# Kernel optimization log

Hardware: AMD Instinct MI355X
Metric: run time of the kernel (lower is better)

Reference implementation:

```python
import jax, jax.numpy as jnp
import numpy as np

E, TOPK, C = 8, 2, 1  # num_local_experts, num_experts_per_tok, num_channels
BS, L, D, F = 8, 1024, 1024, 4096


def setup_inputs() -> dict:
    key = jax.random.key(0)
    ks = jax.random.split(key, 5)
    s = lambda fan_in: 1.0 / np.sqrt(fan_in)
    return {
        "hidden_states": jax.random.normal(ks[0], (BS, L, D), jnp.float32),
        # nn.Linear weight layout [out, in]
        "router_w": jax.random.normal(ks[1], (E, D * C), jnp.float32) * s(D * C),
        "w1": jax.random.normal(ks[2], (E, F, D), jnp.float32) * s(D),
        "w2": jax.random.normal(ks[3], (E, D, F), jnp.float32) * s(F),
        "w3": jax.random.normal(ks[4], (E, F, D), jnp.float32) * s(D),
    }


def _forward(hidden_states, router_w, w1, w2, w3):
    bs, seq, d = hidden_states.shape  # 3D path -> c = 1
    c = C
    h = hidden_states.reshape(bs, seq, c * d)  # [bs, L, c*d]
    # router: per-position logits, then mean over sequence (sentence-level routing)
    router_logits = jnp.einsum('blf,ef->ble', h, router_w).mean(axis=1)  # [bs, E]
    router_probs = jax.nn.softmax(router_logits, axis=-1)
    topk_w, topk_idx = jax.lax.top_k(router_probs, TOPK)  # [bs, TOPK]

    # dense all-expert SwiGLU MLP on every token (as in the original)
    x = h.reshape(bs, seq, c, d)
    outs = []
    for e in range(E):  # fixed small expert count
        up = jnp.einsum('blcd,fd->blcf', x, w1[e])
        gate = jnp.einsum('blcd,fd->blcf', x, w3[e])
        y = jnp.einsum('blcf,df->blcd', jax.nn.silu(up) * gate, w2[e])
        outs.append(y.reshape(bs, seq, c * d))
    expert_outputs = jnp.stack(outs, axis=1)  # [bs, E, L, c*d]

    # Faithful replication of torch.gather(dim=1) with index [bs,L,TOPK,h]:
    # out[b,l,j,:] = expert_outputs[b, topk_idx[b,j], j, :]  (independent of l)
    bi = jnp.arange(bs)[:, None]
    ji = jnp.arange(TOPK)[None, :]
    sel = expert_outputs[bi, topk_idx, ji]  # [bs, TOPK, c*d]
    combined = (sel * topk_w[..., None]).sum(axis=1)  # [bs, c*d]
    out = jnp.broadcast_to(combined[:, None, :], (bs, seq, c * d))
    out = out.reshape(bs, c, seq, d)
    return out, router_logits


def reference(hidden_states, router_w, w1, w2, w3):
    return _forward(hidden_states, router_w, w1, w2, w3)
```

## Files before the change

kernel.cpp:

```cpp
#include <hip/hip_runtime.h>
#include <math.h>

#define BS 8
#define SEQ 1024
#define DIM 1024
#define FF 4096
#define NE 8
#define NSLOT 16
#define MAXM 8
#define NCHUNK 64

#define KS_UG 2
#define KR_UG (DIM / KS_UG)
#define KS_DN 16
#define KR_DN (FF / KS_DN)

#define WS_LPART 0
#define WS_SELW  (WS_LPART + BS*NCHUNK*NE)
#define WS_SELE  (WS_SELW + NSLOT)
#define WS_ACT   (WS_SELE + NSLOT)
#define WS_UPP   (WS_ACT + NSLOT*FF)
#define WS_GTP   (WS_UPP + KS_UG*NSLOT*FF)
#define WS_YP    WS_UPP
#define WS_Y     (WS_GTP + KS_UG*NSLOT*FF)

__device__ __forceinline__ float dot4(float4 a, float4 b) {
    return a.x*b.x + a.y*b.y + a.z*b.z + a.w*b.w;
}

__global__ __launch_bounds__(256) void klogit(const float4* __restrict__ h4,
                                              const float4* __restrict__ rw4,
                                              float* __restrict__ lpart) {
    const int c = blockIdx.x, b = blockIdx.y, t = threadIdx.x;
    const float4* p = h4 + ((size_t)b * SEQ + (size_t)c * 16) * (DIM/4) + t;
    float4 s = make_float4(0.f, 0.f, 0.f, 0.f);
    #pragma unroll
    for (int i = 0; i < 16; ++i) {
        float4 v = p[(size_t)i * (DIM/4)];
        s.x += v.x; s.y += v.y; s.z += v.z; s.w += v.w;
    }
    __shared__ float red[4];
    const int wave = t >> 6, lane = t & 63;
    for (int e = 0; e < NE; ++e) {
        float pd = dot4(s, rw4[(size_t)e * (DIM/4) + t]);
        #pragma unroll
        for (int o = 32; o; o >>= 1) pd += __shfl_xor(pd, o);
        if (lane == 0) red[wave] = pd;
        __syncthreads();
        if (t == 0) lpart[(size_t)(b * NCHUNK + c) * NE + e] = red[0]+red[1]+red[2]+red[3];
        __syncthreads();
    }
}

__global__ void krouter2(const float* __restrict__ lpart,
                         float* __restrict__ out_logits,
                         float* __restrict__ selw, int* __restrict__ sele) {
    const int t = threadIdx.x;
    __shared__ float lg[BS * NE];
    if (t < BS * NE) {
        const int b = t >> 3, e = t & 7;
        float s = 0.f;
        for (int c = 0; c < NCHUNK; ++c) s += lpart[(size_t)(b * NCHUNK + c) * NE + e];
        s *= (1.0f / (float)SEQ);
        lg[b * NE + e] = s;
        out_logits[b * NE + e] = s;
    }
    __syncthreads();
    if (t < BS) {
        float l[NE]; float mx = -1e30f;
        #pragma unroll
        for (int e = 0; e < NE; ++e) { l[e] = lg[t * NE + e]; mx = fmaxf(mx, l[e]); }
        float sum = 0.f;
        #pragma unroll
        for (int e = 0; e < NE; ++e) { l[e] = expf(l[e] - mx); sum += l[e]; }
        const float invs = 1.f / sum;
        float v1 = -1.f, v2 = -1.f; int e1 = -1, e2 = -1;
        #pragma unroll
        for (int e = 0; e < NE; ++e) {
            float pe = l[e] * invs;
            if (pe > v1)      { v2 = v1; e2 = e1; v1 = pe; e1 = e; }
            else if (pe > v2) { v2 = pe; e2 = e; }
        }
        selw[t * 2 + 0] = v1; sele[t * 2 + 0] = e1;
        selw[t * 2 + 1] = v2; sele[t * 2 + 1] = e2;
    }
}

__device__ __forceinline__ int build_slots(const int* __restrict__ sele, int e, int* slot) {
    unsigned mask = 0;
    #pragma unroll
    for (int s = 0; s < NSLOT; ++s) mask |= (sele[s] == e) ? (1u << s) : 0u;
    const int m = __popc(mask);
    unsigned mm = mask;
    #pragma unroll
    for (int ti = 0; ti < MAXM; ++ti) { slot[ti] = __ffs(mm) - 1; mm &= mm - 1; }
    return m;
}

template<int M>
__device__ void ug_body(const float4* __restrict__ wp, const float* __restrict__ xs,
                        float* __restrict__ outp, const int* slot, int row, int sub) {
    float acc[M];
    #pragma unroll
    for (int ti = 0; ti < M; ++ti) acc[ti] = 0.f;
    #pragma unroll 4
    for (int g = 0; g < KR_UG / 16; ++g) {
        float4 w = wp[g * 4];
        #pragma unroll
        for (int ti = 0; ti < M; ++ti) {
            float4 x = *(const float4*)(xs + ti * KR_UG + g * 16 + sub * 4);
            acc[ti] += dot4(w, x);
        }
    }
    #pragma unroll
    for (int ti = 0; ti < M; ++ti) {
        float v = acc[ti];
        v += __shfl_xor(v, 1); v += __shfl_xor(v, 2);
        if (sub == 0) outp[(size_t)slot[ti] * FF + row] = v;
    }
}

__global__ __launch_bounds__(256) void kupgate(const float* __restrict__ h,
                                               const float* __restrict__ w1,
                                               const float* __restrict__ w3,
                                               const int* __restrict__ sele,
                                               float* __restrict__ upp,
                                               float* __restrict__ gtp) {
    __shared__ float xs[MAXM * KR_UG];
    const int tile = blockIdx.x, e = blockIdx.y;
    const int mat = blockIdx.z & 1, ks = blockIdx.z >> 1;
    int slot[MAXM];
    const int m = build_slots(sele, e, slot);
    if (m == 0) return;
    {
        const int ti = threadIdx.x >> 5, j = threadIdx.x & 31;
        if (ti < m) {
            const int s = slot[ti];
            const float4* src = (const float4*)(h
                + ((size_t)((s >> 1) * SEQ + (s & 1))) * DIM + ks * KR_UG);
            float4* dst = (float4*)(xs + ti * KR_UG);
            #pragma unroll
            for (int i = 0; i < KR_UG / 128; ++i) dst[j + i * 32] = src[j + i * 32];
        }
    }
    __syncthreads();
    const int lane = threadIdx.x & 63, wave = threadIdx.x >> 6;
    const int sub = lane & 3;
    const int row = tile * 64 + wave * 16 + (lane >> 2);
    const float* wmat = (mat ? w3 : w1) + (size_t)e * FF * DIM;
    const float4* wp = (const float4*)(wmat + (size_t)row * DIM + ks * KR_UG) + sub;
    float* outp = (mat ? gtp : upp) + (size_t)ks * NSLOT * FF;
    switch (m) {
        case 1: ug_body<1>(wp, xs, outp, slot, row, sub); break;
        case 2: ug_body<2>(wp, xs, outp, slot, row, sub); break;
        case 3: ug_body<3>(wp, xs, outp, slot, row, sub); break;
        case 4: ug_body<4>(wp, xs, outp, slot, row, sub); break;
        case 5: ug_body<5>(wp, xs, outp, slot, row, sub); break;
        case 6: ug_body<6>(wp, xs, outp, slot, row, sub); break;
        case 7: ug_body<7>(wp, xs, outp, slot, row, sub); break;
        default: ug_body<8>(wp, xs, outp, slot, row, sub); break;
    }
}

__global__ __launch_bounds__(256) void kact(const float* __restrict__ upp,
                                            const float* __restrict__ gtp,
                                            float* __restrict__ act) {
    const int r = blockIdx.x * 256 + threadIdx.x, s = blockIdx.y;
    float u = 0.f, g = 0.f;
    #pragma unroll
    for (int ks = 0; ks < KS_UG; ++ks) {
        u += upp[((size_t)ks * NSLOT + s) * FF + r];
        g += gtp[((size_t)ks * NSLOT + s) * FF + r];
    }
    act[(size_t)s * FF + r] = (u / (1.f + expf(-u))) * g;
}

template<int M>
__device__ void dn_body(const float4* __restrict__ wp, const float* __restrict__ xs,
                        float* __restrict__ outp, const int* slot, int row, int sub) {
    float acc[M];
    #pragma unroll
    for (int ti = 0; ti < M; ++ti) acc[ti] = 0.f;
    #pragma unroll 4
    for (int g = 0; g < KR_DN / 16; ++g) {
        float4 w = wp[g * 4];
        #pragma unroll
        for (int ti = 0; ti < M; ++ti) {
            float4 x = *(const float4*)(xs + ti * KR_DN + g * 16 + sub * 4);
            acc[ti] += dot4(w, x);
        }
    }
    #pragma unroll
    for (int ti = 0; ti < M; ++ti) {
        float v = acc[ti];
        v += __shfl_xor(v, 1); v += __shfl_xor(v, 2);
        if (sub == 0) outp[(size_t)slot[ti] * DIM + row] = v;
    }
}

__global__ __launch_bounds__(256) void kdown(const float* __restrict__ w2,
                                             const float* __restrict__ act,
                                             const int* __restrict__ sele,
                                             float* __restrict__ yp) {
    __shared__ float xs[MAXM * KR_DN];
    const int tile = blockIdx.x, e = blockIdx.y, ks = blockIdx.z;
    int slot[MAXM];
    const int m = build_slots(sele, e, slot);
    if (m == 0) return;
    {
        const int ti = threadIdx.x >> 5, j = threadIdx.x & 31;
        if (ti < m) {
            const float4* src = (const float4*)(act + (size_t)slot[ti] * FF + ks * KR_DN);
            float4* dst = (float4*)(xs + ti * KR_DN);
            #pragma unroll
            for (int i = 0; i < KR_DN / 128; ++i) dst[j + i * 32] = src[j + i * 32];
        }
    }
    __syncthreads();
    const int lane = threadIdx.x & 63, wave = threadIdx.x >> 6;
    const int sub = lane & 3;
    const int row = tile * 64 + wave * 16 + (lane >> 2);
    const float4* wp = (const float4*)(w2 + (size_t)e * DIM * FF
                                       + (size_t)row * FF + ks * KR_DN) + sub;
    float* outp = yp + (size_t)ks * NSLOT * DIM;
    switch (m) {
        case 1: dn_body<1>(wp, xs, outp, slot, row, sub); break;
        case 2: dn_body<2>(wp, xs, outp, slot, row, sub); break;
        case 3: dn_body<3>(wp, xs, outp, slot, row, sub); break;
        case 4: dn_body<4>(wp, xs, outp, slot, row, sub); break;
        case 5: dn_body<5>(wp, xs, outp, slot, row, sub); break;
        case 6: dn_body<6>(wp, xs, outp, slot, row, sub); break;
        case 7: dn_body<7>(wp, xs, outp, slot, row, sub); break;
        default: dn_body<8>(wp, xs, outp, slot, row, sub); break;
    }
}

__global__ __launch_bounds__(256) void kcomb(const float* __restrict__ yp,
                                             const float* __restrict__ selw,
                                             float* __restrict__ y) {
    const int r = blockIdx.x * 256 + threadIdx.x, s = blockIdx.y;
    float v = 0.f;
    #pragma unroll
    for (int ks = 0; ks < KS_DN; ++ks)
        v += yp[((size_t)ks * NSLOT + s) * DIM + r];
    y[(size_t)s * DIM + r] = selw[s] * v;
}

__global__ __launch_bounds__(256) void kbcast(const float4* __restrict__ y4,
                                              float4* __restrict__ out4) {
    const int b = blockIdx.y, lg = blockIdx.x, t = threadIdx.x;
    float4 y0 = y4[(size_t)(2 * b) * (DIM/4) + t];
    float4 y1 = y4[(size_t)(2 * b + 1) * (DIM/4) + t];
    float4 c = make_float4(y0.x + y1.x, y0.y + y1.y, y0.z + y1.z, y0.w + y1.w);
    size_t base = ((size_t)b * SEQ + (size_t)lg * 8) * (DIM/4) + t;
    #pragma unroll
    for (int i = 0; i < 8; ++i) out4[base + (size_t)i * (DIM/4)] = c;
}

extern "C" void kernel_launch(void* const* d_in, const int* in_sizes, int n_in,
                              void* d_out, int out_size, void* d_ws, size_t ws_size,
                              hipStream_t stream) {
    const float* h  = (const float*)d_in[0];
    const float* rw = (const float*)d_in[1];
    const float* w1 = (const float*)d_in[2];
    const float* w2 = (const float*)d_in[3];
    const float* w3 = (const float*)d_in[4];
    float* out = (float*)d_out;
    float* ws  = (float*)d_ws;

    float* lpart = ws + WS_LPART;
    float* selw  = ws + WS_SELW;
    int*   sele  = (int*)(ws + WS_SELE);
    float* act   = ws + WS_ACT;
    float* upp   = ws + WS_UPP;
    float* gtp   = ws + WS_GTP;
    float* yp    = ws + WS_YP;
    float* y     = ws + WS_Y;
    float* out_logits = out + (size_t)BS * SEQ * DIM;

    klogit  <<<dim3(NCHUNK, BS), 256, 0, stream>>>((const float4*)h, (const float4*)rw, lpart);
    krouter2<<<1, 64, 0, stream>>>(lpart, out_logits, selw, sele);
    kupgate <<<dim3(FF / 64, NE, 2 * KS_UG), 256, 0, stream>>>(h, w1, w3, sele, upp, gtp);
    kact    <<<dim3(FF / 256, NSLOT), 256, 0, stream>>>(upp, gtp, act);
    kdown   <<<dim3(DIM / 64, NE, KS_DN), 256, 0, stream>>>(w2, act, sele, yp);
    kcomb   <<<dim3(DIM / 256, NSLOT), 256, 0, stream>>>(yp, selw, y);
    kbcast  <<<dim3(SEQ / 8, BS), 256, 0, stream>>>((const float4*)y, (float4*)out);
}
```

Baseline: 120.2 us.

## Fuse up/gate/SiLU into one kernel and drop split-K partials for down projection

Merges the up/gate GEMV, partial reduction and SiLU activation into a single kernel in which each wave owns whole rows of w1 and w3, reduces across the full K dimension and writes the activated value directly. The down projection likewise computes over the full FF dimension inside one block, staging activation chunks through shared memory, and applies the routing weight on output, which removes the separate combine kernel. This removes two launches and the partial-sum workspace round trips, and adds register double-buffering of weight loads. In exchange there are fewer blocks per launch and more work per block, which may reduce memory-level parallelism for these bandwidth-bound weight reads.

```diff
diff --git a/kernel.cpp b/kernel.cpp
--- a/kernel.cpp
+++ b/kernel.cpp
@@ -10,19 +10,11 @@
 #define MAXM 8
 #define NCHUNK 64
 
-#define KS_UG 2
-#define KR_UG (DIM / KS_UG)
-#define KS_DN 16
-#define KR_DN (FF / KS_DN)
-
 #define WS_LPART 0
 #define WS_SELW  (WS_LPART + BS*NCHUNK*NE)
 #define WS_SELE  (WS_SELW + NSLOT)
 #define WS_ACT   (WS_SELE + NSLOT)
-#define WS_UPP   (WS_ACT + NSLOT*FF)
-#define WS_GTP   (WS_UPP + KS_UG*NSLOT*FF)
-#define WS_YP    WS_UPP
-#define WS_Y     (WS_GTP + KS_UG*NSLOT*FF)
+#define WS_Y     (WS_ACT + NSLOT*FF)
 
 __device__ __forceinline__ float dot4(float4 a, float4 b) {
     return a.x*b.x + a.y*b.y + a.z*b.z + a.w*b.w;
@@ -97,153 +89,167 @@
     return m;
 }
 
-template<int M>
-__device__ void ug_body(const float4* __restrict__ wp, const float* __restrict__ xs,
-                        float* __restrict__ outp, const int* slot, int row, int sub) {
-    float acc[M];
-    #pragma unroll
-    for (int ti = 0; ti < M; ++ti) acc[ti] = 0.f;
-    #pragma unroll 4
-    for (int g = 0; g < KR_UG / 16; ++g) {
-        float4 w = wp[g * 4];
-        #pragma unroll
-        for (int ti = 0; ti < M; ++ti) {
-            float4 x = *(const float4*)(xs + ti * KR_UG + g * 16 + sub * 4);
-            acc[ti] += dot4(w, x);
-        }
-    }
-    #pragma unroll
-    for (int ti = 0; ti < M; ++ti) {
-        float v = acc[ti];
-        v += __shfl_xor(v, 1); v += __shfl_xor(v, 2);
-        if (sub == 0) outp[(size_t)slot[ti] * FF + row] = v;
-    }
-}
-
-__global__ __launch_bounds__(256) void kupgate(const float* __restrict__ h,
+#define SW_LD(Ar, Br, R8) {                                            \
+    const size_t rb_ = (size_t)(rowbase + (R8)) * 256 + lane;          \
+    _Pragma("unroll")                                                  \
+    for (int i_ = 0; i_ < 4; ++i_) {                                   \
+        Ar[i_] = w1e4[rb_ + i_ * 64];                                  \
+        Br[i_] = w3e4[rb_ + i_ * 64];                                  \
+    } }
+
+template<int MM>
+__device__ void swiglu_body(const float4* __restrict__ w1e4,
+                            const float4* __restrict__ w3e4,
+                            const float4* __restrict__ xs4,
+                            float* __restrict__ act,
+                            const int* slot, int m, int rowbase, int lane) {
+    float4 A0[4], B0[4], A1[4], B1[4];
+    SW_LD(A0, B0, 0)
+    for (int r8 = 0; r8 < 8; r8 += 2) {
+        SW_LD(A1, B1, r8 + 1)
+        {
+            const int row = rowbase + r8;
+            #pragma unroll
+            for (int ti = 0; ti < MM; ++ti) {
+                float u = 0.f, g = 0.f;
+                #pragma unroll
+                for (int i = 0; i < 4; ++i) {
+                    float4 x = xs4[ti * 256 + i * 64 + lane];
+                    u += dot4(A0[i], x); g += dot4(B0[i], x);
+                }
+                #pragma unroll
+                for (int o = 32; o; o >>= 1) { u += __shfl_xor(u, o); g += __shfl_xor(g, o); }
+                if (ti < m && lane == 0)
+                    act[(size_t)slot[ti] * FF + row] = (u / (1.f + expf(-u))) * g;
+            }
+        }
+        if (r8 + 2 < 8) SW_LD(A0, B0, r8 + 2)
+        {
+            const int row = rowbase + r8 + 1;
+            #pragma unroll
+            for (int ti = 0; ti < MM; ++ti) {
+                float u = 0.f, g = 0.f;
+                #pragma unroll
+                for (int i = 0; i < 4; ++i) {
+                    float4 x = xs4[ti * 256 + i * 64 + lane];
+                    u += dot4(A1[i], x); g += dot4(B1[i], x);
+                }
+                #pragma unroll
+                for (int o = 32; o; o >>= 1) { u += __shfl_xor(u, o); g += __shfl_xor(g, o); }
+                if (ti < m && lane == 0)
+                    act[(size_t)slot[ti] * FF + row] = (u / (1.f + expf(-u))) * g;
+            }
+        }
+    }
+}
+
+__global__ __launch_bounds__(256) void kswiglu(const float* __restrict__ h,
                                                const float* __restrict__ w1,
                                                const float* __restrict__ w3,
                                                const int* __restrict__ sele,
-                                               float* __restrict__ upp,
-                                               float* __restrict__ gtp) {
-    __shared__ float xs[MAXM * KR_UG];
-    const int tile = blockIdx.x, e = blockIdx.y;
-    const int mat = blockIdx.z & 1, ks = blockIdx.z >> 1;
+                                               float* __restrict__ act) {
+    __shared__ float xs[MAXM * DIM];
+    const int tile = blockIdx.x, e = blockIdx.y, t = threadIdx.x;
     int slot[MAXM];
     const int m = build_slots(sele, e, slot);
     if (m == 0) return;
     {
-        const int ti = threadIdx.x >> 5, j = threadIdx.x & 31;
+        const int ti = t >> 5, j = t & 31;
+        float4* dst = (float4*)(xs + ti * DIM);
         if (ti < m) {
             const int s = slot[ti];
-            const float4* src = (const float4*)(h
-                + ((size_t)((s >> 1) * SEQ + (s & 1))) * DIM + ks * KR_UG);
-            float4* dst = (float4*)(xs + ti * KR_UG);
-            #pragma unroll
-            for (int i = 0; i < KR_UG / 128; ++i) dst[j + i * 32] = src[j + i * 32];
+            const float4* src = (const float4*)(h + ((size_t)((s >> 1) * SEQ + (s & 1))) * DIM);
+            #pragma unroll
+            for (int i = 0; i < 8; ++i) dst[j + i * 32] = src[j + i * 32];
+        } else {
+            const float4 z = make_float4(0.f, 0.f, 0.f, 0.f);
+            #pragma unroll
+            for (int i = 0; i < 8; ++i) dst[j + i * 32] = z;
         }
     }
     __syncthreads();
-    const int lane = threadIdx.x & 63, wave = threadIdx.x >> 6;
-    const int sub = lane & 3;
-    const int row = tile * 64 + wave * 16 + (lane >> 2);
-    const float* wmat = (mat ? w3 : w1) + (size_t)e * FF * DIM;
-    const float4* wp = (const float4*)(wmat + (size_t)row * DIM + ks * KR_UG) + sub;
-    float* outp = (mat ? gtp : upp) + (size_t)ks * NSLOT * FF;
-    switch (m) {
-        case 1: ug_body<1>(wp, xs, outp, slot, row, sub); break;
-        case 2: ug_body<2>(wp, xs, outp, slot, row, sub); break;
-        case 3: ug_body<3>(wp, xs, outp, slot, row, sub); break;
-        case 4: ug_body<4>(wp, xs, outp, slot, row, sub); break;
-        case 5: ug_body<5>(wp, xs, outp, slot, row, sub); break;
-        case 6: ug_body<6>(wp, xs, outp, slot, row, sub); break;
-        case 7: ug_body<7>(wp, xs, outp, slot, row, sub); break;
-        default: ug_body<8>(wp, xs, outp, slot, row, sub); break;
-    }
-}
-
-__global__ __launch_bounds__(256) void kact(const float* __restrict__ upp,
-                                            const float* __restrict__ gtp,
-                                            float* __restrict__ act) {
-    const int r = blockIdx.x * 256 + threadIdx.x, s = blockIdx.y;
-    float u = 0.f, g = 0.f;
-    #pragma unroll
-    for (int ks = 0; ks < KS_UG; ++ks) {
-        u += upp[((size_t)ks * NSLOT + s) * FF + r];
-        g += gtp[((size_t)ks * NSLOT + s) * FF + r];
-    }
-    act[(size_t)s * FF + r] = (u / (1.f + expf(-u))) * g;
-}
-
-template<int M>
-__device__ void dn_body(const float4* __restrict__ wp, const float* __restrict__ xs,
-                        float* __restrict__ outp, const int* slot, int row, int sub) {
-    float acc[M];
-    #pragma unroll
-    for (int ti = 0; ti < M; ++ti) acc[ti] = 0.f;
-    #pragma unroll 4
-    for (int g = 0; g < KR_DN / 16; ++g) {
-        float4 w = wp[g * 4];
-        #pragma unroll
-        for (int ti = 0; ti < M; ++ti) {
-            float4 x = *(const float4*)(xs + ti * KR_DN + g * 16 + sub * 4);
-            acc[ti] += dot4(w, x);
-        }
-    }
-    #pragma unroll
-    for (int ti = 0; ti < M; ++ti) {
-        float v = acc[ti];
-        v += __shfl_xor(v, 1); v += __shfl_xor(v, 2);
-        if (sub == 0) outp[(size_t)slot[ti] * DIM + row] = v;
+    const int wave = t >> 6, lane = t & 63;
+    const int rowbase = tile * 32 + wave * 8;
+    const float4* w1e4 = (const float4*)w1 + (size_t)e * FF * (DIM/4);
+    const float4* w3e4 = (const float4*)w3 + (size_t)e * FF * (DIM/4);
+    if (m <= 4) swiglu_body<4>(w1e4, w3e4, (const float4*)xs, act, slot, m, rowbase, lane);
+    else        swiglu_body<8>(w1e4, w3e4, (const float4*)xs, act, slot, m, rowbase, lane);
+}
+
+template<int MM>
+__device__ void down_body(const float4* __restrict__ w2e4,
+                          const float* __restrict__ act,
+                          const float* __restrict__ selw,
+                          float* __restrict__ y,
+                          const int* slot, int m, int tile, int t, float* xs) {
+    const int wave = t >> 6, lane = t & 63;
+    const int rowbase = tile * 16 + wave * 4;
+    float acc[4][MM];
+    #pragma unroll
+    for (int r = 0; r < 4; ++r)
+        #pragma unroll
+        for (int ti = 0; ti < MM; ++ti) acc[r][ti] = 0.f;
+
+    for (int c = 0; c < 4; ++c) {
+        __syncthreads();
+        {
+            const int ti = t >> 5, j = t & 31;
+            float4* dst = (float4*)(xs + ti * 1024);
+            if (ti < m) {
+                const float4* src = (const float4*)(act + (size_t)slot[ti] * FF + c * 1024);
+                #pragma unroll
+                for (int i = 0; i < 8; ++i) dst[j + i * 32] = src[j + i * 32];
+            } else {
+                const float4 z = make_float4(0.f, 0.f, 0.f, 0.f);
+                #pragma unroll
+                for (int i = 0; i < 8; ++i) dst[j + i * 32] = z;
+            }
+        }
+        __syncthreads();
+        float4 W[4][4];
+        #pragma unroll
+        for (int r = 0; r < 4; ++r) {
+            const size_t rb = (size_t)(rowbase + r) * (FF/4) + c * 256 + lane;
+            #pragma unroll
+            for (int i = 0; i < 4; ++i) W[r][i] = w2e4[rb + i * 64];
+        }
+        const float4* xs4 = (const float4*)xs;
+        #pragma unroll
+        for (int i = 0; i < 4; ++i) {
+            #pragma unroll
+            for (int ti = 0; ti < MM; ++ti) {
+                float4 x = xs4[ti * 256 + i * 64 + lane];
+                #pragma unroll
+                for (int r = 0; r < 4; ++r) acc[r][ti] += dot4(W[r][i], x);
+            }
+        }
+    }
+    #pragma unroll
+    for (int r = 0; r < 4; ++r) {
+        #pragma unroll
+        for (int ti = 0; ti < MM; ++ti) {
+            float v = acc[r][ti];
+            #pragma unroll
+            for (int o = 32; o; o >>= 1) v += __shfl_xor(v, o);
+            if (ti < m && lane == 0)
+                y[(size_t)slot[ti] * DIM + rowbase + r] = selw[slot[ti]] * v;
+        }
     }
 }
 
 __global__ __launch_bounds__(256) void kdown(const float* __restrict__ w2,
                                              const float* __restrict__ act,
                                              const int* __restrict__ sele,
-                                             float* __restrict__ yp) {
-    __shared__ float xs[MAXM * KR_DN];
-    const int tile = blockIdx.x, e = blockIdx.y, ks = blockIdx.z;
+                                             const float* __restrict__ selw,
+                                             float* __restrict__ y) {
+    __shared__ float xs[MAXM * 1024];
+    const int tile = blockIdx.x, e = blockIdx.y, t = threadIdx.x;
     int slot[MAXM];
     const int m = build_slots(sele, e, slot);
     if (m == 0) return;
-    {
-        const int ti = threadIdx.x >> 5, j = threadIdx.x & 31;
-        if (ti < m) {
-            const float4* src = (const float4*)(act + (size_t)slot[ti] * FF + ks * KR_DN);
-            float4* dst = (float4*)(xs + ti * KR_DN);
-            #pragma unroll
-            for (int i = 0; i < KR_DN / 128; ++i) dst[j + i * 32] = src[j + i * 32];
-        }
-    }
-    __syncthreads();
-    const int lane = threadIdx.x & 63, wave = threadIdx.x >> 6;
-    const int sub = lane & 3;
-    const int row = tile * 64 + wave * 16 + (lane >> 2);
-    const float4* wp = (const float4*)(w2 + (size_t)e * DIM * FF
-                                       + (size_t)row * FF + ks * KR_DN) + sub;
-    float* outp = yp + (size_t)ks * NSLOT * DIM;
-    switch (m) {
-        case 1: dn_body<1>(wp, xs, outp, slot, row, sub); break;
-        case 2: dn_body<2>(wp, xs, outp, slot, row, sub); break;
-        case 3: dn_body<3>(wp, xs, outp, slot, row, sub); break;
-        case 4: dn_body<4>(wp, xs, outp, slot, row, sub); break;
-        case 5: dn_body<5>(wp, xs, outp, slot, row, sub); break;
-        case 6: dn_body<6>(wp, xs, outp, slot, row, sub); break;
-        case 7: dn_body<7>(wp, xs, outp, slot, row, sub); break;
-        default: dn_body<8>(wp, xs, outp, slot, row, sub); break;
-    }
-}
-
-__global__ __launch_bounds__(256) void kcomb(const float* __restrict__ yp,
-                                             const float* __restrict__ selw,
-                                             float* __restrict__ y) {
-    const int r = blockIdx.x * 256 + threadIdx.x, s = blockIdx.y;
-    float v = 0.f;
-    #pragma unroll
-    for (int ks = 0; ks < KS_DN; ++ks)
-        v += yp[((size_t)ks * NSLOT + s) * DIM + r];
-    y[(size_t)s * DIM + r] = selw[s] * v;
+    const float4* w2e4 = (const float4*)w2 + (size_t)e * DIM * (FF/4);
+    if (m <= 4) down_body<4>(w2e4, act, selw, y, slot, m, tile, t, xs);
+    else        down_body<8>(w2e4, act, selw, y, slot, m, tile, t, xs);
 }
 
 __global__ __launch_bounds__(256) void kbcast(const float4* __restrict__ y4,
@@ -272,17 +278,12 @@
     float* selw  = ws + WS_SELW;
     int*   sele  = (int*)(ws + WS_SELE);
     float* act   = ws + WS_ACT;
-    float* upp   = ws + WS_UPP;
-    float* gtp   = ws + WS_GTP;
-    float* yp    = ws + WS_YP;
     float* y     = ws + WS_Y;
     float* out_logits = out + (size_t)BS * SEQ * DIM;
 
     klogit  <<<dim3(NCHUNK, BS), 256, 0, stream>>>((const float4*)h, (const float4*)rw, lpart);
     krouter2<<<1, 64, 0, stream>>>(lpart, out_logits, selw, sele);
-    kupgate <<<dim3(FF / 64, NE, 2 * KS_UG), 256, 0, stream>>>(h, w1, w3, sele, upp, gtp);
-    kact    <<<dim3(FF / 256, NSLOT), 256, 0, stream>>>(upp, gtp, act);
-    kdown   <<<dim3(DIM / 64, NE, KS_DN), 256, 0, stream>>>(w2, act, sele, yp);
-    kcomb   <<<dim3(DIM / 256, NSLOT), 256, 0, stream>>>(yp, selw, y);
+    kswiglu <<<dim3(FF / 32, NE), 256, 0, stream>>>(h, w1, w3, sele, act);
+    kdown   <<<dim3(DIM / 16, NE), 256, 0, stream>>>(w2, act, sele, selw, y);
     kbcast  <<<dim3(SEQ / 8, BS), 256, 0, stream>>>((const float4*)y, (float4*)out);
 }
```

Measured after the change: 127.1 us. 5.7% more time.

## Fuse up/gate GEMV, map one weight row per thread, batch router reductions

Applied to the files above, without the earlier changes.

The up and gate projections are merged into one kernel, so each block streams both w1 and w3 rows and reuses the staged token vectors held in shared memory. Both GEMV kernels switch from four lanes sharing a row to one full row per thread, which removes the cross-lane shuffle reduction. They also collapse the eight templated slot counts into two variants (4 and 8), and the up/gate K-split goes from 2 to 4. The router logit kernel now reduces all eight experts together with one barrier instead of two barriers per expert. The costs are that adjacent lanes now read weight rows a full row apart, which loses coalescing, and that padded slots do wasted FMAs when m is not 4 or 8.

```diff
diff --git a/kernel.cpp b/kernel.cpp
--- a/kernel.cpp
+++ b/kernel.cpp
@@ -10,10 +10,10 @@
 #define MAXM 8
 #define NCHUNK 64
 
-#define KS_UG 2
-#define KR_UG (DIM / KS_UG)
+#define KS_UG 4
+#define KC_UG (DIM / KS_UG)
 #define KS_DN 16
-#define KR_DN (FF / KS_DN)
+#define KC_DN (FF / KS_DN)
 
 #define WS_LPART 0
 #define WS_SELW  (WS_LPART + BS*NCHUNK*NE)
@@ -39,17 +39,24 @@
         float4 v = p[(size_t)i * (DIM/4)];
         s.x += v.x; s.y += v.y; s.z += v.z; s.w += v.w;
     }
-    __shared__ float red[4];
+    float pd[NE];
+    #pragma unroll
+    for (int e = 0; e < NE; ++e) pd[e] = dot4(s, rw4[(size_t)e * (DIM/4) + t]);
+    #pragma unroll
+    for (int o = 32; o; o >>= 1) {
+        #pragma unroll
+        for (int e = 0; e < NE; ++e) pd[e] += __shfl_xor(pd[e], o);
+    }
+    __shared__ float red[4][NE];
     const int wave = t >> 6, lane = t & 63;
-    for (int e = 0; e < NE; ++e) {
-        float pd = dot4(s, rw4[(size_t)e * (DIM/4) + t]);
-        #pragma unroll
-        for (int o = 32; o; o >>= 1) pd += __shfl_xor(pd, o);
-        if (lane == 0) red[wave] = pd;
-        __syncthreads();
-        if (t == 0) lpart[(size_t)(b * NCHUNK + c) * NE + e] = red[0]+red[1]+red[2]+red[3];
-        __syncthreads();
-    }
+    if (lane == 0) {
+        #pragma unroll
+        for (int e = 0; e < NE; ++e) red[wave][e] = pd[e];
+    }
+    __syncthreads();
+    if (t < NE)
+        lpart[(size_t)(b * NCHUNK + c) * NE + t] =
+            red[0][t] + red[1][t] + red[2][t] + red[3][t];
 }
 
 __global__ void krouter2(const float* __restrict__ lpart,
@@ -97,69 +104,89 @@
     return m;
 }
 
-template<int M>
-__device__ void ug_body(const float4* __restrict__ wp, const float* __restrict__ xs,
-                        float* __restrict__ outp, const int* slot, int row, int sub) {
-    float acc[M];
-    #pragma unroll
-    for (int ti = 0; ti < M; ++ti) acc[ti] = 0.f;
-    #pragma unroll 4
-    for (int g = 0; g < KR_UG / 16; ++g) {
-        float4 w = wp[g * 4];
-        #pragma unroll
-        for (int ti = 0; ti < M; ++ti) {
-            float4 x = *(const float4*)(xs + ti * KR_UG + g * 16 + sub * 4);
-            acc[ti] += dot4(w, x);
-        }
-    }
-    #pragma unroll
-    for (int ti = 0; ti < M; ++ti) {
-        float v = acc[ti];
-        v += __shfl_xor(v, 1); v += __shfl_xor(v, 2);
-        if (sub == 0) outp[(size_t)slot[ti] * FF + row] = v;
-    }
-}
-
-__global__ __launch_bounds__(256) void kupgate(const float* __restrict__ h,
+__device__ __forceinline__ void slots_to_lds(const int* __restrict__ sele, int e,
+                                             int t, int* sslot) {
+    if (t < MAXM) {
+        unsigned mask = 0;
+        #pragma unroll
+        for (int s = 0; s < NSLOT; ++s) mask |= (sele[s] == e) ? (1u << s) : 0u;
+        unsigned mm = mask; int sl = -1;
+        for (int k = 0; k <= t; ++k) { sl = __ffs(mm) - 1; mm &= mm - 1; }
+        sslot[t] = sl;
+    }
+}
+
+template<int MM>
+__device__ void swiglu_body(const float4* __restrict__ w1p,
+                            const float4* __restrict__ w3p,
+                            const float4* __restrict__ xs4,
+                            float* __restrict__ up_out, float* __restrict__ gt_out,
+                            const int* slot, int m, int row) {
+    float ua[MM], ga[MM];
+    #pragma unroll
+    for (int ti = 0; ti < MM; ++ti) { ua[ti] = 0.f; ga[ti] = 0.f; }
+    for (int c = 0; c < KC_UG / 16; ++c) {
+        float4 W1[4], W3[4];
+        #pragma unroll
+        for (int i = 0; i < 4; ++i) W1[i] = w1p[c * 4 + i];
+        #pragma unroll
+        for (int i = 0; i < 4; ++i) W3[i] = w3p[c * 4 + i];
+        #pragma unroll
+        for (int i = 0; i < 4; ++i) {
+            #pragma unroll
+            for (int ti = 0; ti < MM; ++ti) {
+                float4 x = xs4[ti * (KC_UG/4) + c * 4 + i];
+                ua[ti] += dot4(W1[i], x);
+                ga[ti] += dot4(W3[i], x);
+            }
+        }
+    }
+    #pragma unroll
+    for (int ti = 0; ti < MM; ++ti) {
+        if (ti < m) {
+            up_out[(size_t)slot[ti] * FF + row] = ua[ti];
+            gt_out[(size_t)slot[ti] * FF + row] = ga[ti];
+        }
+    }
+}
+
+__global__ __launch_bounds__(256) void kswiglu(const float* __restrict__ h,
                                                const float* __restrict__ w1,
                                                const float* __restrict__ w3,
                                                const int* __restrict__ sele,
                                                float* __restrict__ upp,
                                                float* __restrict__ gtp) {
-    __shared__ float xs[MAXM * KR_UG];
-    const int tile = blockIdx.x, e = blockIdx.y;
-    const int mat = blockIdx.z & 1, ks = blockIdx.z >> 1;
+    __shared__ float xs[MAXM * KC_UG];
+    __shared__ int sslot[MAXM];
+    const int tile = blockIdx.x, e = blockIdx.y, ks = blockIdx.z, t = threadIdx.x;
     int slot[MAXM];
     const int m = build_slots(sele, e, slot);
     if (m == 0) return;
+    slots_to_lds(sele, e, t, sslot);
+    __syncthreads();
     {
-        const int ti = threadIdx.x >> 5, j = threadIdx.x & 31;
-        if (ti < m) {
-            const int s = slot[ti];
-            const float4* src = (const float4*)(h
-                + ((size_t)((s >> 1) * SEQ + (s & 1))) * DIM + ks * KR_UG);
-            float4* dst = (float4*)(xs + ti * KR_UG);
-            #pragma unroll
-            for (int i = 0; i < KR_UG / 128; ++i) dst[j + i * 32] = src[j + i * 32];
-        }
-    }
-    __syncthreads();
-    const int lane = threadIdx.x & 63, wave = threadIdx.x >> 6;
-    const int sub = lane & 3;
-    const int row = tile * 64 + wave * 16 + (lane >> 2);
-    const float* wmat = (mat ? w3 : w1) + (size_t)e * FF * DIM;
-    const float4* wp = (const float4*)(wmat + (size_t)row * DIM + ks * KR_UG) + sub;
-    float* outp = (mat ? gtp : upp) + (size_t)ks * NSLOT * FF;
-    switch (m) {
-        case 1: ug_body<1>(wp, xs, outp, slot, row, sub); break;
-        case 2: ug_body<2>(wp, xs, outp, slot, row, sub); break;
-        case 3: ug_body<3>(wp, xs, outp, slot, row, sub); break;
-        case 4: ug_body<4>(wp, xs, outp, slot, row, sub); break;
-        case 5: ug_body<5>(wp, xs, outp, slot, row, sub); break;
-        case 6: ug_body<6>(wp, xs, outp, slot, row, sub); break;
-        case 7: ug_body<7>(wp, xs, outp, slot, row, sub); break;
-        default: ug_body<8>(wp, xs, outp, slot, row, sub); break;
-    }
+        float4* xs4 = (float4*)xs;
+        const float4* h4 = (const float4*)h;
+        #pragma unroll
+        for (int q = 0; q < 2; ++q) {
+            const int idx = t + q * 256;
+            const int ti = idx >> 6, j = idx & 63;
+            const int s = sslot[ti];
+            float4 v = make_float4(0.f, 0.f, 0.f, 0.f);
+            if (ti < m)
+                v = h4[((size_t)((s >> 1) * SEQ + (s & 1))) * (DIM/4) + ks * (KC_UG/4) + j];
+            xs4[idx] = v;
+        }
+    }
+    __syncthreads();
+    const int wave = t >> 6, lane = t & 63;
+    const int row = tile * 256 + wave * 64 + lane;
+    const float4* w1p = (const float4*)w1 + ((size_t)e * FF + row) * (DIM/4) + ks * (KC_UG/4);
+    const float4* w3p = (const float4*)w3 + ((size_t)e * FF + row) * (DIM/4) + ks * (KC_UG/4);
+    float* up_out = upp + (size_t)ks * NSLOT * FF;
+    float* gt_out = gtp + (size_t)ks * NSLOT * FF;
+    if (m <= 4) swiglu_body<4>(w1p, w3p, (const float4*)xs, up_out, gt_out, slot, m, row);
+    else        swiglu_body<8>(w1p, w3p, (const float4*)xs, up_out, gt_out, slot, m, row);
 }
 
 __global__ __launch_bounds__(256) void kact(const float* __restrict__ upp,
@@ -175,69 +202,69 @@
     act[(size_t)s * FF + r] = (u / (1.f + expf(-u))) * g;
 }
 
-template<int M>
-__device__ void dn_body(const float4* __restrict__ wp, const float* __restrict__ xs,
-                        float* __restrict__ outp, const int* slot, int row, int sub) {
-    float acc[M];
-    #pragma unroll
-    for (int ti = 0; ti < M; ++ti) acc[ti] = 0.f;
-    #pragma unroll 4
-    for (int g = 0; g < KR_DN / 16; ++g) {
-        float4 w = wp[g * 4];
-        #pragma unroll
-        for (int ti = 0; ti < M; ++ti) {
-            float4 x = *(const float4*)(xs + ti * KR_DN + g * 16 + sub * 4);
-            acc[ti] += dot4(w, x);
-        }
-    }
-    #pragma unroll
-    for (int ti = 0; ti < M; ++ti) {
-        float v = acc[ti];
-        v += __shfl_xor(v, 1); v += __shfl_xor(v, 2);
-        if (sub == 0) outp[(size_t)slot[ti] * DIM + row] = v;
-    }
+template<int MM>
+__device__ void down_body(const float4* __restrict__ wp,
+                          const float4* __restrict__ xs4,
+                          float* __restrict__ y_out,
+                          const int* slot, int m, int row) {
+    float acc[MM];
+    #pragma unroll
+    for (int ti = 0; ti < MM; ++ti) acc[ti] = 0.f;
+    for (int c = 0; c < KC_DN / 16; ++c) {
+        float4 W[4];
+        #pragma unroll
+        for (int i = 0; i < 4; ++i) W[i] = wp[c * 4 + i];
+        #pragma unroll
+        for (int i = 0; i < 4; ++i) {
+            #pragma unroll
+            for (int ti = 0; ti < MM; ++ti) {
+                float4 x = xs4[ti * (KC_DN/4) + c * 4 + i];
+                acc[ti] += dot4(W[i], x);
+            }
+        }
+    }
+    #pragma unroll
+    for (int ti = 0; ti < MM; ++ti)
+        if (ti < m) y_out[(size_t)slot[ti] * DIM + row] = acc[ti];
 }
 
 __global__ __launch_bounds__(256) void kdown(const float* __restrict__ w2,
                                              const float* __restrict__ act,
                                              const int* __restrict__ sele,
                                              float* __restrict__ yp) {
-    __shared__ float xs[MAXM * KR_DN];
-    const int tile = blockIdx.x, e = blockIdx.y, ks = blockIdx.z;
+    __shared__ float xs[MAXM * KC_DN];
+    __shared__ int sslot[MAXM];
+    const int tile = blockIdx.x, e = blockIdx.y, ks = blockIdx.z, t = threadIdx.x;
     int slot[MAXM];
     const int m = build_slots(sele, e, slot);
     if (m == 0) return;
+    slots_to_lds(sele, e, t, sslot);
+    __syncthreads();
     {
-        const int ti = threadIdx.x >> 5, j = threadIdx.x & 31;
-        if (ti < m) {
-            const float4* src = (const float4*)(act + (size_t)slot[ti] * FF + ks * KR_DN);
-            float4* dst = (float4*)(xs + ti * KR_DN);
-            #pragma unroll
-            for (int i = 0; i < KR_DN / 128; ++i) dst[j + i * 32] = src[j + i * 32];
-        }
-    }
-    __syncthreads();
-    const int lane = threadIdx.x & 63, wave = threadIdx.x >> 6;
-    const int sub = lane & 3;
-    const int row = tile * 64 + wave * 16 + (lane >> 2);
-    const float4* wp = (const float4*)(w2 + (size_t)e * DIM * FF
-                                       + (size_t)row * FF + ks * KR_DN) + sub;
-    float* outp = yp + (size_t)ks * NSLOT * DIM;
-    switch (m) {
-        case 1: dn_body<1>(wp, xs, outp, slot, row, sub); break;
-        case 2: dn_body<2>(wp, xs, outp, slot, row, sub); break;
-        case 3: dn_body<3>(wp, xs, outp, slot, row, sub); break;
-        case 4: dn_body<4>(wp, xs, outp, slot, row, sub); break;
-        case 5: dn_body<5>(wp, xs, outp, slot, row, sub); break;
-        case 6: dn_body<6>(wp, xs, outp, slot, row, sub); break;
-        case 7: dn_body<7>(wp, xs, outp, slot, row, sub); break;
-        default: dn_body<8>(wp, xs, outp, slot, row, sub); break;
-    }
-}
-
-__global__ __launch_bounds__(256) void kcomb(const float* __restrict__ yp,
-                                             const float* __restrict__ selw,
-                                             float* __restrict__ y) {
+        float4* xs4 = (float4*)xs;
+        const float4* a4 = (const float4*)act;
+        #pragma unroll
+        for (int q = 0; q < 2; ++q) {
+            const int idx = t + q * 256;
+            const int ti = idx >> 6, j = idx & 63;
+            const int s = sslot[ti];
+            float4 v = make_float4(0.f, 0.f, 0.f, 0.f);
+            if (ti < m) v = a4[(size_t)s * (FF/4) + ks * (KC_DN/4) + j];
+            xs4[idx] = v;
+        }
+    }
+    __syncthreads();
+    const int wave = t >> 6, lane = t & 63;
+    const int row = tile * 256 + wave * 64 + lane;
+    const float4* wp = (const float4*)w2 + ((size_t)e * DIM + row) * (FF/4) + ks * (KC_DN/4);
+    float* y_out = yp + (size_t)ks * NSLOT * DIM;
+    if (m <= 4) down_body<4>(wp, (const float4*)xs, y_out, slot, m, row);
+    else        down_body<8>(wp, (const float4*)xs, y_out, slot, m, row);
+}
+
+__global__ __launch_bounds__(256) void kcomby(const float* __restrict__ yp,
+                                              const float* __restrict__ selw,
+                                              float* __restrict__ y) {
     const int r = blockIdx.x * 256 + threadIdx.x, s = blockIdx.y;
     float v = 0.f;
     #pragma unroll
@@ -280,9 +307,9 @@
 
     klogit  <<<dim3(NCHUNK, BS), 256, 0, stream>>>((const float4*)h, (const float4*)rw, lpart);
     krouter2<<<1, 64, 0, stream>>>(lpart, out_logits, selw, sele);
-    kupgate <<<dim3(FF / 64, NE, 2 * KS_UG), 256, 0, stream>>>(h, w1, w3, sele, upp, gtp);
+    kswiglu <<<dim3(FF / 256, NE, KS_UG), 256, 0, stream>>>(h, w1, w3, sele, upp, gtp);
     kact    <<<dim3(FF / 256, NSLOT), 256, 0, stream>>>(upp, gtp, act);
-    kdown   <<<dim3(DIM / 64, NE, KS_DN), 256, 0, stream>>>(w2, act, sele, yp);
-    kcomb   <<<dim3(DIM / 256, NSLOT), 256, 0, stream>>>(yp, selw, y);
+    kdown   <<<dim3(DIM / 256, NE, KS_DN), 256, 0, stream>>>(w2, act, sele, yp);
+    kcomby  <<<dim3(DIM / 256, NSLOT), 256, 0, stream>>>(yp, selw, y);
     kbcast  <<<dim3(SEQ / 8, BS), 256, 0, stream>>>((const float4*)y, (float4*)out);
 }
```

Result: slower. 157.8 us (+31.3%).
